# Performance work log

Hardware: AMD Instinct MI355X
Metric: run time of the kernel (lower is better)

The kernel has to match this reference:

```python
import jax, jax.numpy as jnp
import numpy as np

EPS = 1e-5


def _layernorm(x, w, b):
    mu = jnp.mean(x, axis=-1, keepdims=True)
    var = jnp.var(x, axis=-1, keepdims=True)
    return (x - mu) * jax.lax.rsqrt(var + EPS) * w + b


def setup_inputs() -> dict:
    key = jax.random.key(0)
    ks = jax.random.split(key, 3)
    h, dff = 1024, 4096
    x = jax.random.normal(ks[0], (4, 2048, h), dtype=jnp.float32)
    w1 = jax.random.normal(ks[1], (h, dff), dtype=jnp.float32) * (1.0 / np.sqrt(h))
    w2 = jax.random.normal(ks[2], (dff, h), dtype=jnp.float32) * (1.0 / np.sqrt(dff))
    return {
        "x": x,
        "ln1_w": jnp.ones((h,), jnp.float32),
        "ln1_b": jnp.zeros((h,), jnp.float32),
        "ln2_w": jnp.ones((h,), jnp.float32),
        "ln2_b": jnp.zeros((h,), jnp.float32),
        "w1": w1,
        "b1": jnp.zeros((dff,), jnp.float32),
        "w2": w2,
        "b2": jnp.zeros((h,), jnp.float32),
    }


def reference(x, ln1_w, ln1_b, ln2_w, ln2_b, w1, b1, w2, b2):
    # double 1D FFT: over hidden (dim=-1) then sequence (dim=-2), keep real part
    fourier_x = jnp.fft.fft(jnp.fft.fft(x, axis=-1), axis=-2).real
    x = x + fourier_x
    x = _layernorm(x, ln1_w, ln1_b)
    # FFN: Linear -> exact GELU -> Linear (dropout is identity in eval)
    h = jax.nn.gelu(jnp.einsum("bsd,df->bsf", x, w1) + b1, approximate=False)
    x = x + jnp.einsum("bsf,fd->bsd", h, w2) + b2
    return _layernorm(x, ln2_w, ln2_b)
```

## Files before the change

### kernel.cpp

```cpp
#include <hip/hip_runtime.h>
#include <hip/hip_bf16.h>
#include <math.h>

typedef __bf16 bf16_t;
typedef __bf16 bf16x8 __attribute__((ext_vector_type(8)));
typedef __bf16 bf16x4 __attribute__((ext_vector_type(4)));
typedef float  f32x4  __attribute__((ext_vector_type(4)));

#define NROWS 8192
#define HD    1024
#define DFF   4096
#define HKEEP 513

typedef __attribute__((address_space(1))) const void* gas_cptr;
typedef __attribute__((address_space(3))) void* las_ptr;

__device__ __forceinline__ void gload_lds16(const void* g, void* l) {
  __builtin_amdgcn_global_load_lds((gas_cptr)g, (las_ptr)l, 16, 0, 0);
}

__global__ __launch_bounds__(256) void transpose_to_bf16(
    const float* __restrict__ in, bf16_t* __restrict__ out, int R, int C)
{
  __shared__ float tile[32][33];
  const int bx = blockIdx.x, by = blockIdx.y;
  const int tx = threadIdx.x, ty = threadIdx.y;
  #pragma unroll
  for (int i = ty; i < 32; i += 8)
    tile[i][tx] = in[(size_t)(by*32 + i)*C + bx*32 + tx];
  __syncthreads();
  #pragma unroll
  for (int i = ty; i < 32; i += 8)
    out[(size_t)(bx*32 + i)*R + by*32 + tx] = (bf16_t)tile[tx][i];
}

#define RPB 16
#define LDW 1036
__global__ __launch_bounds__(512) void fft_h_t(
    const float* __restrict__ x, float* __restrict__ reT, float* __restrict__ imT)
{
  __shared__ float sre[RPB*LDW], sim[RPB*LDW], twc[512], tws[512];
  const int t = threadIdx.x;
  const int row0 = blockIdx.x * RPB;
  {
    float sv, cv; sincosf(-6.28318530717958647692f * (float)t * (1.0f/1024.0f), &sv, &cv);
    twc[t] = cv; tws[t] = sv;
  }
  #pragma unroll
  for (int q = 0; q < 8; ++q) {
    const int i = t + 512*q;
    const int row = i >> 8, c4 = i & 255;
    float4 v = *(const float4*)(x + (size_t)(row0+row)*HD + c4*4);
    *(float4*)&sre[row*LDW + c4*4] = v;
  }
  __syncthreads();
  const int b0i = __brev((unsigned)t) >> 22;
  const int b1i = __brev((unsigned)(t + 512)) >> 22;
  float rv[32];
  #pragma unroll
  for (int q = 0; q < 16; ++q) {
    rv[2*q]   = sre[q*LDW + b0i];
    rv[2*q+1] = sre[q*LDW + b1i];
  }
  __syncthreads();
  #pragma unroll
  for (int q = 0; q < 16; ++q) {
    sre[q*LDW + t]       = rv[2*q];
    sre[q*LDW + t + 512] = rv[2*q+1];
    sim[q*LDW + t]       = 0.0f;
    sim[q*LDW + t + 512] = 0.0f;
  }
  __syncthreads();
  for (int s = 0; s < 10; ++s) {
    const int half = 1 << s;
    const int j    = t & (half - 1);
    const int ib   = ((t >> s) << (s + 1)) | j;
    const int ti2  = j << (9 - s);
    const float wc = twc[ti2], ws = tws[ti2];
    #pragma unroll
    for (int q = 0; q < 16; ++q) {
      float* pr = &sre[q*LDW]; float* pi = &sim[q*LDW];
      const float r1 = pr[ib],      i1v = pi[ib];
      const float r2 = pr[ib+half], i2v = pi[ib+half];
      const float tr = r2*wc - i2v*ws;
      const float ti = r2*ws + i2v*wc;
      pr[ib]      = r1 + tr; pi[ib]      = i1v + ti;
      pr[ib+half] = r1 - tr; pi[ib+half] = i1v - ti;
    }
    __syncthreads();
  }
  const int tx = t & 15, th = t >> 4;
  #pragma unroll
  for (int hh = 0; hh < 17; ++hh) {
    const int h = hh*32 + th;
    if (h < HKEEP) {
      reT[(size_t)h*NROWS + row0 + tx] = sre[tx*LDW + h];
      imT[(size_t)h*NROWS + row0 + tx] = sim[tx*LDW + h];
    }
  }
}

__global__ __launch_bounds__(256) void fft_s_col(
    const float* __restrict__ reT, const float* __restrict__ imT,
    float* __restrict__ fT)
{
  __shared__ float sre[2048], sim[2048], twc[1024], tws[1024];
  const int t = threadIdx.x;
  const int h = blockIdx.x;
  const int batch = blockIdx.y;
  const size_t base = (size_t)h * NROWS + batch * 2048;
  for (int k = t; k < 1024; k += 256) {
    float sv, cv; sincosf(-6.28318530717958647692f * (float)k * (1.0f/2048.0f), &sv, &cv);
    twc[k] = cv; tws[k] = sv;
  }
  #pragma unroll
  for (int q = 0; q < 8; ++q) {
    const int i = t + 256*q;
    const int src = __brev((unsigned)i) >> 21;
    sre[i] = reT[base + src];
    sim[i] = imT[base + src];
  }
  __syncthreads();
  for (int s = 0; s < 11; ++s) {
    const int half = 1 << s;
    #pragma unroll
    for (int q = 0; q < 4; ++q) {
      const int b  = t + 256*q;
      const int j  = b & (half - 1);
      const int ib = ((b >> s) << (s + 1)) | j;
      const int ti2 = j << (10 - s);
      const float wc = twc[ti2], ws = tws[ti2];
      const float r1 = sre[ib],       i1v = sim[ib];
      const float r2 = sre[ib+half],  i2v = sim[ib+half];
      const float tr = r2*wc - i2v*ws;
      const float ti = r2*ws + i2v*wc;
      sre[ib]      = r1 + tr; sim[ib]      = i1v + ti;
      sre[ib+half] = r1 - tr; sim[ib+half] = i1v - ti;
    }
    __syncthreads();
  }
  #pragma unroll
  for (int q = 0; q < 8; ++q) {
    const int i = t + 256*q;
    fT[base + i] = sre[i];
  }
}

__global__ __launch_bounds__(256) void umadd_kernel(
    const float* __restrict__ fT, const float* __restrict__ x,
    float* __restrict__ y)
{
  __shared__ float tile[32][33];
  const int h0 = blockIdx.x * 32;
  const int b0 = blockIdx.y * 32;
  const int tx = threadIdx.x, ty = threadIdx.y;
  const int batch = b0 >> 11;
  const int s0    = b0 & 2047;
  #pragma unroll
  for (int i = ty; i < 32; i += 8) {
    const int h = h0 + i;
    float v;
    if (h <= 512) {
      v = fT[(size_t)h * NROWS + b0 + tx];
    } else {
      const int sp = (2048 - (s0 + tx)) & 2047;
      v = fT[(size_t)(1024 - h) * NROWS + (batch << 11) + sp];
    }
    tile[i][tx] = v;
  }
  __syncthreads();
  #pragma unroll
  for (int i = ty; i < 32; i += 8) {
    const size_t gi = (size_t)(b0+i)*HD + h0+tx;
    y[gi] = x[gi] + tile[tx][i];
  }
}

template <bool OUT_BF16>
__global__ __launch_bounds__(256) void layernorm_k(
    const float* __restrict__ in, const float* __restrict__ gw,
    const float* __restrict__ gb, bf16_t* __restrict__ ob, float* __restrict__ of)
{
  __shared__ float red[8];
  const size_t row = blockIdx.x;
  const int t = threadIdx.x;
  const float* xr = in + row * HD;
  float4 v = *(const float4*)(xr + t*4);
  float s = v.x + v.y + v.z + v.w;
  #pragma unroll
  for (int o = 32; o > 0; o >>= 1) s += __shfl_xor(s, o);
  if ((t & 63) == 0) red[t >> 6] = s;
  __syncthreads();
  const float mu = (red[0]+red[1]+red[2]+red[3]) * (1.0f/1024.0f);
  const float dx = v.x-mu, dy = v.y-mu, dz = v.z-mu, dw = v.w-mu;
  float sq = dx*dx + dy*dy + dz*dz + dw*dw;
  #pragma unroll
  for (int o = 32; o > 0; o >>= 1) sq += __shfl_xor(sq, o);
  if ((t & 63) == 0) red[4 + (t >> 6)] = sq;
  __syncthreads();
  const float var  = (red[4]+red[5]+red[6]+red[7]) * (1.0f/1024.0f);
  const float rstd = rsqrtf(var + 1e-5f);
  const float4 wv = *(const float4*)(gw + t*4);
  const float4 bv = *(const float4*)(gb + t*4);
  const float o0 = dx*rstd*wv.x + bv.x;
  const float o1 = dy*rstd*wv.y + bv.y;
  const float o2 = dz*rstd*wv.z + bv.z;
  const float o3 = dw*rstd*wv.w + bv.w;
  if constexpr (OUT_BF16) {
    bf16x4 o; o[0]=(bf16_t)o0; o[1]=(bf16_t)o1; o[2]=(bf16_t)o2; o[3]=(bf16_t)o3;
    *(bf16x4*)(ob + row*HD + t*4) = o;
  } else {
    float4 o; o.x=o0; o.y=o1; o.z=o2; o.w=o3;
    *(float4*)(of + row*HD + t*4) = o;
  }
}

__device__ __forceinline__ float gelu_fast(float v) {
  const float u  = 0.7978845608028654f * v * (1.0f + 0.044715f * v * v);
  const float e  = exp2f(-2.8853900817779268f * u);
  return v / (1.0f + e);
}

template <bool GELU_BF16_OUT>
__global__ __launch_bounds__(256) void gemm_bf16_kernel(
    const bf16_t* __restrict__ A,
    const bf16_t* __restrict__ Bt,
    const float*  __restrict__ bias,
    const bf16_t* __restrict__ resid,
    bf16_t* __restrict__ outB, float* __restrict__ outF,
    int M, int N, int K, int gx)
{
  constexpr int BK = 64;
  __shared__ bf16_t As[128*BK];
  __shared__ bf16_t Bs[128*BK];
  const int tid  = threadIdx.x;
  const int wave = tid >> 6, lane = tid & 63;
  const int wr = wave >> 1, wc = wave & 1;
  const int lr  = lane & 15;
  const int lkg = lane >> 4;

  const int nwg = gridDim.x;
  const int sid = (blockIdx.x & 7) * (nwg >> 3) + (blockIdx.x >> 3);
  const int bx = sid % gx, by = sid / gx;
  const int brow = by * 128, bcol = bx * 128;

  const int rloc = lane >> 3;
  const int sgrp = (lane & 7) ^ rloc;
  const bf16_t* Ag = A  + (size_t)(brow + wave*32 + rloc) * K + sgrp * 8;
  const bf16_t* Bg = Bt + (size_t)(bcol + wave*32 + rloc) * K + sgrp * 8;

  f32x4 acc[4][4] = {};

  for (int k0 = 0; k0 < K; k0 += BK) {
    #pragma unroll
    for (int q = 0; q < 4; ++q) {
      gload_lds16(Ag + (size_t)(q*8)*K + k0, &As[(wave*4 + q) * 512]);
      gload_lds16(Bg + (size_t)(q*8)*K + k0, &Bs[(wave*4 + q) * 512]);
    }
    __syncthreads();

    #pragma unroll
    for (int ks = 0; ks < 2; ++ks) {
      const int g = (lkg + ks*4) ^ (lr & 7);
      bf16x8 af[4], bv[4];
      #pragma unroll
      for (int m = 0; m < 4; ++m)
        af[m] = *(const bf16x8*)&As[(wr*64 + m*16 + lr)*BK + g*8];
      #pragma unroll
      for (int n = 0; n < 4; ++n)
        bv[n] = *(const bf16x8*)&Bs[(wc*64 + n*16 + lr)*BK + g*8];
      #pragma unroll
      for (int m = 0; m < 4; ++m)
        #pragma unroll
        for (int n = 0; n < 4; ++n)
          acc[m][n] = __builtin_amdgcn_mfma_f32_16x16x32_bf16(bv[n], af[m], acc[m][n], 0, 0, 0);
    }
    __syncthreads();
  }

  #pragma unroll
  for (int m = 0; m < 4; ++m) {
    const int row = brow + wr*64 + m*16 + lr;
    #pragma unroll
    for (int n = 0; n < 4; ++n) {
      const int col = bcol + wc*64 + n*16 + lkg*4;
      const float4 bv4 = *(const float4*)(bias + col);
      float v0 = acc[m][n][0] + bv4.x;
      float v1 = acc[m][n][1] + bv4.y;
      float v2 = acc[m][n][2] + bv4.z;
      float v3 = acc[m][n][3] + bv4.w;
      if constexpr (GELU_BF16_OUT) {
        bf16x4 o;
        o[0] = (bf16_t)gelu_fast(v0); o[1] = (bf16_t)gelu_fast(v1);
        o[2] = (bf16_t)gelu_fast(v2); o[3] = (bf16_t)gelu_fast(v3);
        *(bf16x4*)(outB + (size_t)row * N + col) = o;
      } else {
        bf16x4 rr = *(const bf16x4*)(resid + (size_t)row * N + col);
        float4 o;
        o.x = v0 + (float)rr[0]; o.y = v1 + (float)rr[1];
        o.z = v2 + (float)rr[2]; o.w = v3 + (float)rr[3];
        *(float4*)(outF + (size_t)row * N + col) = o;
      }
    }
  }
}

extern "C" void kernel_launch(void* const* d_in, const int* in_sizes, int n_in,
                              void* d_out, int out_size, void* d_ws, size_t ws_size,
                              hipStream_t stream) {
  const float* x    = (const float*)d_in[0];
  const float* ln1w = (const float*)d_in[1];
  const float* ln1b = (const float*)d_in[2];
  const float* ln2w = (const float*)d_in[3];
  const float* ln2b = (const float*)d_in[4];
  const float* w1   = (const float*)d_in[5];
  const float* b1   = (const float*)d_in[6];
  const float* w2   = (const float*)d_in[7];
  const float* b2   = (const float*)d_in[8];
  float* out = (float*)d_out;

  char* ws = (char*)d_ws;
  bf16_t* w1b = (bf16_t*)(ws);
  bf16_t* w2b = (bf16_t*)(ws + (8u  << 20));
  float*  reT = (float*) (ws + (16u << 20));
  float*  imT = (float*) (ws + (33u << 20));
  float*  fT  = (float*) (ws + (50u << 20));
  float*  y   = (float*) (ws + (67u << 20));
  bf16_t* xn  = (bf16_t*)(ws + (99u << 20));
  bf16_t* hg  = (bf16_t*)(ws + (16u << 20));

  transpose_to_bf16<<<dim3(DFF/32, HD/32), dim3(32, 8), 0, stream>>>(w1, w1b, HD, DFF);
  transpose_to_bf16<<<dim3(HD/32, DFF/32), dim3(32, 8), 0, stream>>>(w2, w2b, DFF, HD);

  fft_h_t<<<NROWS/RPB, 512, 0, stream>>>(x, reT, imT);

  fft_s_col<<<dim3(513, 4), 256, 0, stream>>>(reT, imT, fT);

  umadd_kernel<<<dim3(HD/32, NROWS/32), dim3(32, 8), 0, stream>>>(fT, x, y);

  layernorm_k<true><<<NROWS, 256, 0, stream>>>(y, ln1w, ln1b, xn, nullptr);

  gemm_bf16_kernel<true><<<(DFF/128)*(NROWS/128), 256, 0, stream>>>(
      xn, w1b, b1, nullptr, hg, nullptr, NROWS, DFF, HD, DFF/128);
  gemm_bf16_kernel<false><<<(HD/128)*(NROWS/128), 256, 0, stream>>>(
      hg, w2b, b2, xn, nullptr, out, NROWS, HD, DFF, HD/128);

  layernorm_k<false><<<NROWS, 256, 0, stream>>>(out, ln2w, ln2b, nullptr, out);
}
```

Measured before the change: 326.9 us.

## Pipeline GEMMs with 8-wave 256-row tiles and fuse residual add into LN1

Replaces the 128x128 single-buffered GEMM with a 512-thread, 256-row tile kernel. It double-buffers LDS and splits each K tile into eight phases that interleave global-to-LDS prefetch with MFMA, using explicit vmcnt waits, barriers and setprio. Separately, it fuses the Fourier-term transpose and residual add with LayerNorm1 into one kernel that holds 16 rows in LDS, removing the fp32 y round trip. The risks are larger LDS and register use per block, hand-tuned wait counts that must match the load issue order, and a single-pass variance (E[x²]−μ²) that is less numerically stable.

```diff
diff --git a/kernel.cpp b/kernel.cpp
--- a/kernel.cpp
+++ b/kernel.cpp
@@ -17,6 +17,14 @@
 
 __device__ __forceinline__ void gload_lds16(const void* g, void* l) {
   __builtin_amdgcn_global_load_lds((gas_cptr)g, (las_ptr)l, 16, 0, 0);
+}
+
+template <int N> __device__ __forceinline__ void vmw() {
+  if      constexpr (N==3) asm volatile("s_waitcnt vmcnt(3)" ::: "memory");
+  else if constexpr (N==4) asm volatile("s_waitcnt vmcnt(4)" ::: "memory");
+  else if constexpr (N==5) asm volatile("s_waitcnt vmcnt(5)" ::: "memory");
+  else if constexpr (N==6) asm volatile("s_waitcnt vmcnt(6)" ::: "memory");
+  else if constexpr (N==8) asm volatile("s_waitcnt vmcnt(8)" ::: "memory");
 }
 
 __global__ __launch_bounds__(256) void transpose_to_bf16(
@@ -146,40 +154,73 @@
   }
 }
 
-__global__ __launch_bounds__(256) void umadd_kernel(
+#define FLD 1028
+__global__ __launch_bounds__(256) void fuse_umadd_ln1(
     const float* __restrict__ fT, const float* __restrict__ x,
-    float* __restrict__ y)
-{
-  __shared__ float tile[32][33];
-  const int h0 = blockIdx.x * 32;
-  const int b0 = blockIdx.y * 32;
-  const int tx = threadIdx.x, ty = threadIdx.y;
-  const int batch = b0 >> 11;
-  const int s0    = b0 & 2047;
-  #pragma unroll
-  for (int i = ty; i < 32; i += 8) {
-    const int h = h0 + i;
+    const float* __restrict__ gw, const float* __restrict__ gb,
+    bf16_t* __restrict__ xn)
+{
+  __shared__ float tile[16*FLD];
+  __shared__ float mrow[16], vrow[16];
+  const int t = threadIdx.x;
+  const int r0 = blockIdx.x * 16;
+  const int batch = r0 >> 11;
+  const int rb = t & 15;
+  const int hh = t >> 4;
+  const int rloc = (r0 + rb) & 2047;
+  const int sp = (2048 - rloc) & 2047;
+  #pragma unroll
+  for (int p = 0; p < 64; ++p) {
+    const int h = p*16 + hh;
     float v;
-    if (h <= 512) {
-      v = fT[(size_t)h * NROWS + b0 + tx];
-    } else {
-      const int sp = (2048 - (s0 + tx)) & 2047;
-      v = fT[(size_t)(1024 - h) * NROWS + (batch << 11) + sp];
-    }
-    tile[i][tx] = v;
-  }
-  __syncthreads();
-  #pragma unroll
-  for (int i = ty; i < 32; i += 8) {
-    const size_t gi = (size_t)(b0+i)*HD + h0+tx;
-    y[gi] = x[gi] + tile[tx][i];
-  }
-}
-
-template <bool OUT_BF16>
-__global__ __launch_bounds__(256) void layernorm_k(
+    if (h <= 512) v = fT[(size_t)h*NROWS + r0 + rb];
+    else          v = fT[(size_t)(1024-h)*NROWS + (batch<<11) + sp];
+    tile[rb*FLD + h] = v;
+  }
+  __syncthreads();
+  #pragma unroll
+  for (int rr = 0; rr < 16; ++rr) {
+    float4 xv = *(const float4*)(x + (size_t)(r0+rr)*HD + t*4);
+    float4 tv = *(float4*)&tile[rr*FLD + t*4];
+    tv.x += xv.x; tv.y += xv.y; tv.z += xv.z; tv.w += xv.w;
+    *(float4*)&tile[rr*FLD + t*4] = tv;
+  }
+  __syncthreads();
+  {
+    const int r = t >> 4, i = t & 15;
+    float s = 0.f, s2 = 0.f;
+    #pragma unroll
+    for (int k = 0; k < 64; ++k) {
+      const float v = tile[r*FLD + i + 16*k];
+      s += v; s2 += v*v;
+    }
+    #pragma unroll
+    for (int o = 8; o > 0; o >>= 1) { s += __shfl_xor(s, o); s2 += __shfl_xor(s2, o); }
+    if (i == 0) {
+      const float mu = s * (1.0f/1024.0f);
+      mrow[r] = mu;
+      vrow[r] = rsqrtf(s2 * (1.0f/1024.0f) - mu*mu + 1e-5f);
+    }
+  }
+  __syncthreads();
+  const float4 wv = *(const float4*)(gw + t*4);
+  const float4 bv = *(const float4*)(gb + t*4);
+  #pragma unroll
+  for (int rr = 0; rr < 16; ++rr) {
+    const float mu = mrow[rr], rs = vrow[rr];
+    float4 tv = *(float4*)&tile[rr*FLD + t*4];
+    bf16x4 o;
+    o[0] = (bf16_t)((tv.x-mu)*rs*wv.x + bv.x);
+    o[1] = (bf16_t)((tv.y-mu)*rs*wv.y + bv.y);
+    o[2] = (bf16_t)((tv.z-mu)*rs*wv.z + bv.z);
+    o[3] = (bf16_t)((tv.w-mu)*rs*wv.w + bv.w);
+    *(bf16x4*)(xn + (size_t)(r0+rr)*HD + t*4) = o;
+  }
+}
+
+__global__ __launch_bounds__(256) void layernorm_f32(
     const float* __restrict__ in, const float* __restrict__ gw,
-    const float* __restrict__ gb, bf16_t* __restrict__ ob, float* __restrict__ of)
+    const float* __restrict__ gb, float* __restrict__ of)
 {
   __shared__ float red[8];
   const size_t row = blockIdx.x;
@@ -202,17 +243,12 @@
   const float rstd = rsqrtf(var + 1e-5f);
   const float4 wv = *(const float4*)(gw + t*4);
   const float4 bv = *(const float4*)(gb + t*4);
-  const float o0 = dx*rstd*wv.x + bv.x;
-  const float o1 = dy*rstd*wv.y + bv.y;
-  const float o2 = dz*rstd*wv.z + bv.z;
-  const float o3 = dw*rstd*wv.w + bv.w;
-  if constexpr (OUT_BF16) {
-    bf16x4 o; o[0]=(bf16_t)o0; o[1]=(bf16_t)o1; o[2]=(bf16_t)o2; o[3]=(bf16_t)o3;
-    *(bf16x4*)(ob + row*HD + t*4) = o;
-  } else {
-    float4 o; o.x=o0; o.y=o1; o.z=o2; o.w=o3;
-    *(float4*)(of + row*HD + t*4) = o;
-  }
+  float4 o;
+  o.x = dx*rstd*wv.x + bv.x;
+  o.y = dy*rstd*wv.y + bv.y;
+  o.z = dz*rstd*wv.z + bv.z;
+  o.w = dw*rstd*wv.w + bv.w;
+  *(float4*)(of + row*HD + t*4) = o;
 }
 
 __device__ __forceinline__ float gelu_fast(float v) {
@@ -221,8 +257,8 @@
   return v / (1.0f + e);
 }
 
-template <bool GELU_BF16_OUT>
-__global__ __launch_bounds__(256) void gemm_bf16_kernel(
+template <int NQ, bool GELU_OUT>
+__global__ __launch_bounds__(512, 2) void gemm8p(
     const bf16_t* __restrict__ A,
     const bf16_t* __restrict__ Bt,
     const float*  __restrict__ bias,
@@ -230,66 +266,104 @@
     bf16_t* __restrict__ outB, float* __restrict__ outF,
     int M, int N, int K, int gx)
 {
-  constexpr int BK = 64;
-  __shared__ bf16_t As[128*BK];
-  __shared__ bf16_t Bs[128*BK];
+  constexpr int S  = NQ * 16;
+  constexpr int WA = (NQ==2) ? 6 : 5;
+  constexpr int WB = (NQ==2) ? 8 : 6;
+  constexpr int WP = (NQ==2) ? 4 : 3;
+  __shared__ bf16_t As[2][2][128*64];
+  __shared__ bf16_t Bs[2][2][NQ*64*64];
+
   const int tid  = threadIdx.x;
   const int wave = tid >> 6, lane = tid & 63;
-  const int wr = wave >> 1, wc = wave & 1;
-  const int lr  = lane & 15;
-  const int lkg = lane >> 4;
+  const int wr = wave >> 2, wc = wave & 3;
+  const int lr = lane & 15, lkg = lane >> 4;
 
   const int nwg = gridDim.x;
   const int sid = (blockIdx.x & 7) * (nwg >> 3) + (blockIdx.x >> 3);
   const int bx = sid % gx, by = sid / gx;
-  const int brow = by * 128, bcol = bx * 128;
-
-  const int rloc = lane >> 3;
-  const int sgrp = (lane & 7) ^ rloc;
-  const bf16_t* Ag = A  + (size_t)(brow + wave*32 + rloc) * K + sgrp * 8;
-  const bf16_t* Bg = Bt + (size_t)(bcol + wave*32 + rloc) * K + sgrp * 8;
-
-  f32x4 acc[4][4] = {};
-
-  for (int k0 = 0; k0 < K; k0 += BK) {
-    #pragma unroll
-    for (int q = 0; q < 4; ++q) {
-      gload_lds16(Ag + (size_t)(q*8)*K + k0, &As[(wave*4 + q) * 512]);
-      gload_lds16(Bg + (size_t)(q*8)*K + k0, &Bs[(wave*4 + q) * 512]);
-    }
-    __syncthreads();
-
-    #pragma unroll
-    for (int ks = 0; ks < 2; ++ks) {
-      const int g = (lkg + ks*4) ^ (lr & 7);
-      bf16x8 af[4], bv[4];
-      #pragma unroll
-      for (int m = 0; m < 4; ++m)
-        af[m] = *(const bf16x8*)&As[(wr*64 + m*16 + lr)*BK + g*8];
-      #pragma unroll
-      for (int n = 0; n < 4; ++n)
-        bv[n] = *(const bf16x8*)&Bs[(wc*64 + n*16 + lr)*BK + g*8];
-      #pragma unroll
-      for (int m = 0; m < 4; ++m)
-        #pragma unroll
-        for (int n = 0; n < 4; ++n)
-          acc[m][n] = __builtin_amdgcn_mfma_f32_16x16x32_bf16(bv[n], af[m], acc[m][n], 0, 0, 0);
-    }
-    __syncthreads();
-  }
-
-  #pragma unroll
-  for (int m = 0; m < 4; ++m) {
-    const int row = brow + wr*64 + m*16 + lr;
-    #pragma unroll
-    for (int n = 0; n < 4; ++n) {
-      const int col = bcol + wc*64 + n*16 + lkg*4;
+  const int brow = by * 256, bcol = bx * (NQ*128);
+
+  const int rl = lane >> 3;
+  const int sg = (lane & 7) ^ rl;
+
+  auto stageA = [&](int b, int mh, int tt) {
+    #pragma unroll
+    for (int l = 0; l < 2; ++l) {
+      const int row = brow + l*128 + mh*64 + wave*8 + rl;
+      gload_lds16(A + (size_t)row * K + tt*64 + sg*8,
+                  &As[b][mh][(l*64 + wave*8)*64]);
+    }
+  };
+  auto stageB = [&](int b, int nh, int tt) {
+    #pragma unroll
+    for (int l = 0; l < NQ; ++l) {
+      const int rho = l*64 + wave*8 + rl;
+      const int wcs = rho / S, r = rho % S;
+      const int row = bcol + wcs*2*S + nh*S + r;
+      gload_lds16(Bt + (size_t)row * K + tt*64 + sg*8,
+                  &Bs[b][nh][(l*64 + wave*8)*64]);
+    }
+  };
+
+  f32x4 acc[8][2*NQ] = {};
+
+  const int NT = K >> 6;
+  const int NI = NT >> 1;
+
+  stageA(0,0,0); stageB(0,0,0); stageA(0,1,0); stageB(0,1,0);
+  stageA(1,0,1); stageB(1,0,1);
+  vmw<WP>();
+  __builtin_amdgcn_s_barrier();
+
+  #define PHASE(BUF, MH, NH, STG, WN) do { \
+    bf16x8 af[4][2]; bf16x8 bq[NQ][2]; \
+    _Pragma("unroll") for (int m = 0; m < 4; ++m) \
+    _Pragma("unroll") for (int ks = 0; ks < 2; ++ks) \
+      af[m][ks] = *(const bf16x8*)&As[BUF][MH][(wr*64 + m*16 + lr)*64 + (((lkg + ks*4) ^ (lr & 7)) << 3)]; \
+    _Pragma("unroll") for (int n = 0; n < NQ; ++n) \
+    _Pragma("unroll") for (int ks = 0; ks < 2; ++ks) \
+      bq[n][ks] = *(const bf16x8*)&Bs[BUF][NH][(wc*S + n*16 + lr)*64 + (((lkg + ks*4) ^ (lr & 7)) << 3)]; \
+    STG; \
+    __builtin_amdgcn_s_barrier(); \
+    asm volatile("s_waitcnt lgkmcnt(0)" ::: "memory"); \
+    __builtin_amdgcn_sched_barrier(0); \
+    __builtin_amdgcn_s_setprio(1); \
+    _Pragma("unroll") for (int m = 0; m < 4; ++m) \
+    _Pragma("unroll") for (int n = 0; n < NQ; ++n) \
+    _Pragma("unroll") for (int ks = 0; ks < 2; ++ks) \
+      acc[MH*4 + m][NH*NQ + n] = __builtin_amdgcn_mfma_f32_16x16x32_bf16(bq[n][ks], af[m][ks], acc[MH*4 + m][NH*NQ + n], 0, 0, 0); \
+    __builtin_amdgcn_s_setprio(0); \
+    vmw<WN>(); \
+    __builtin_amdgcn_s_barrier(); \
+  } while (0)
+
+  for (int j = 0; j < NI; ++j) {
+    const int c1 = 2*j + 1;
+    const int n2 = (2*j + 2 < NT) ? 2*j + 2 : NT - 1;
+    const int n3 = (2*j + 3 < NT) ? 2*j + 3 : NT - 1;
+    PHASE(0,0,0, stageA(1,1,c1), WA);
+    PHASE(0,0,1, stageB(1,1,c1), 63);
+    PHASE(0,1,0, stageA(0,0,n2), 63);
+    PHASE(0,1,1, stageB(0,0,n2), WB);
+    PHASE(1,0,0, stageA(0,1,n2), WA);
+    PHASE(1,0,1, stageB(0,1,n2), 63);
+    PHASE(1,1,0, stageA(1,0,n3), 63);
+    PHASE(1,1,1, stageB(1,0,n3), WB);
+  }
+  #undef PHASE
+
+  #pragma unroll
+  for (int im = 0; im < 8; ++im) {
+    const int row = brow + wr*128 + (im >> 2)*64 + (im & 3)*16 + lr;
+    #pragma unroll
+    for (int in = 0; in < 2*NQ; ++in) {
+      const int col = bcol + wc*2*S + (in/NQ)*S + (in%NQ)*16 + lkg*4;
       const float4 bv4 = *(const float4*)(bias + col);
-      float v0 = acc[m][n][0] + bv4.x;
-      float v1 = acc[m][n][1] + bv4.y;
-      float v2 = acc[m][n][2] + bv4.z;
-      float v3 = acc[m][n][3] + bv4.w;
-      if constexpr (GELU_BF16_OUT) {
+      float v0 = acc[im][in][0] + bv4.x;
+      float v1 = acc[im][in][1] + bv4.y;
+      float v2 = acc[im][in][2] + bv4.z;
+      float v3 = acc[im][in][3] + bv4.w;
+      if constexpr (GELU_OUT) {
         bf16x4 o;
         o[0] = (bf16_t)gelu_fast(v0); o[1] = (bf16_t)gelu_fast(v1);
         o[2] = (bf16_t)gelu_fast(v2); o[3] = (bf16_t)gelu_fast(v3);
@@ -321,13 +395,12 @@
 
   char* ws = (char*)d_ws;
   bf16_t* w1b = (bf16_t*)(ws);
-  bf16_t* w2b = (bf16_t*)(ws + (8u  << 20));
-  float*  reT = (float*) (ws + (16u << 20));
-  float*  imT = (float*) (ws + (33u << 20));
-  float*  fT  = (float*) (ws + (50u << 20));
-  float*  y   = (float*) (ws + (67u << 20));
-  bf16_t* xn  = (bf16_t*)(ws + (99u << 20));
-  bf16_t* hg  = (bf16_t*)(ws + (16u << 20));
+  bf16_t* w2b = (bf16_t*)(ws + (8u   << 20));
+  float*  reT = (float*) (ws + (16u  << 20));
+  float*  imT = (float*) (ws + (33u  << 20));
+  float*  fT  = (float*) (ws + (50u  << 20));
+  bf16_t* xn  = (bf16_t*)(ws + (100u << 20));
+  bf16_t* hg  = (bf16_t*)(ws + (16u  << 20));
 
   transpose_to_bf16<<<dim3(DFF/32, HD/32), dim3(32, 8), 0, stream>>>(w1, w1b, HD, DFF);
   transpose_to_bf16<<<dim3(HD/32, DFF/32), dim3(32, 8), 0, stream>>>(w2, w2b, DFF, HD);
@@ -336,14 +409,12 @@
 
   fft_s_col<<<dim3(513, 4), 256, 0, stream>>>(reT, imT, fT);
 
-  umadd_kernel<<<dim3(HD/32, NROWS/32), dim3(32, 8), 0, stream>>>(fT, x, y);
-
-  layernorm_k<true><<<NROWS, 256, 0, stream>>>(y, ln1w, ln1b, xn, nullptr);
-
-  gemm_bf16_kernel<true><<<(DFF/128)*(NROWS/128), 256, 0, stream>>>(
-      xn, w1b, b1, nullptr, hg, nullptr, NROWS, DFF, HD, DFF/128);
-  gemm_bf16_kernel<false><<<(HD/128)*(NROWS/128), 256, 0, stream>>>(
+  fuse_umadd_ln1<<<NROWS/16, 256, 0, stream>>>(fT, x, ln1w, ln1b, xn);
+
+  gemm8p<2, true><<<(NROWS/256)*(DFF/256), 512, 0, stream>>>(
+      xn, w1b, b1, nullptr, hg, nullptr, NROWS, DFF, HD, DFF/256);
+  gemm8p<1, false><<<(NROWS/256)*(HD/128), 512, 0, stream>>>(
       hg, w2b, b2, xn, nullptr, out, NROWS, HD, DFF, HD/128);
 
-  layernorm_k<false><<<NROWS, 256, 0, stream>>>(out, ln2w, ln2b, nullptr, out);
-}
+  layernorm_f32<<<NROWS, 256, 0, stream>>>(out, ln2w, ln2b, out);
+}
```

New measurement: 334.4 us. +2.3%, slower.

## Rewrite FFN GEMMs as 8-wave double-buffered pipelined kernel with larger tiles

Applied to the files above, without the earlier changes.

Replaces the 128x128 single-buffered bf16 GEMM with an 8-wave (512-thread) kernel using 256x256 (first GEMM) or 256x128 (second GEMM) tiles. It splits LDS into double-buffered half-tiles and interleaves global-to-LDS loads with MFMA phases, using explicit vmcnt waits, barriers and setprio. The goal is to hide memory latency behind MFMA work and raise data reuse per tile. It adds heavy LDS use and register pressure (64 or 32 accumulators per lane), and the hand-tuned wait counts risk races if they are wrong.

```diff
diff --git a/kernel.cpp b/kernel.cpp
--- a/kernel.cpp
+++ b/kernel.cpp
@@ -17,6 +17,14 @@
 
 __device__ __forceinline__ void gload_lds16(const void* g, void* l) {
   __builtin_amdgcn_global_load_lds((gas_cptr)g, (las_ptr)l, 16, 0, 0);
+}
+
+template <int N> __device__ __forceinline__ void vmw() {
+  if      constexpr (N==4)  asm volatile("s_waitcnt vmcnt(4)"  ::: "memory");
+  else if constexpr (N==6)  asm volatile("s_waitcnt vmcnt(6)"  ::: "memory");
+  else if constexpr (N==7)  asm volatile("s_waitcnt vmcnt(7)"  ::: "memory");
+  else if constexpr (N==8)  asm volatile("s_waitcnt vmcnt(8)"  ::: "memory");
+  else if constexpr (N==10) asm volatile("s_waitcnt vmcnt(10)" ::: "memory");
 }
 
 __global__ __launch_bounds__(256) void transpose_to_bf16(
@@ -221,8 +229,8 @@
   return v / (1.0f + e);
 }
 
-template <bool GELU_BF16_OUT>
-__global__ __launch_bounds__(256) void gemm_bf16_kernel(
+template <int NQ, bool GELU_OUT>
+__global__ __launch_bounds__(512, 2) void gemm8r(
     const bf16_t* __restrict__ A,
     const bf16_t* __restrict__ Bt,
     const float*  __restrict__ bias,
@@ -230,66 +238,112 @@
     bf16_t* __restrict__ outB, float* __restrict__ outF,
     int M, int N, int K, int gx)
 {
-  constexpr int BK = 64;
-  __shared__ bf16_t As[128*BK];
-  __shared__ bf16_t Bs[128*BK];
+  __shared__ bf16_t As[2][2][128*64];
+  __shared__ bf16_t Bs[2][2][NQ*64*64];
+
   const int tid  = threadIdx.x;
   const int wave = tid >> 6, lane = tid & 63;
-  const int wr = wave >> 1, wc = wave & 1;
-  const int lr  = lane & 15;
-  const int lkg = lane >> 4;
+  const int wr = wave >> 2, wc = wave & 3;
+  const int lr = lane & 15, lkg = lane >> 4;
 
   const int nwg = gridDim.x;
   const int sid = (blockIdx.x & 7) * (nwg >> 3) + (blockIdx.x >> 3);
   const int bx = sid % gx, by = sid / gx;
-  const int brow = by * 128, bcol = bx * 128;
-
-  const int rloc = lane >> 3;
-  const int sgrp = (lane & 7) ^ rloc;
-  const bf16_t* Ag = A  + (size_t)(brow + wave*32 + rloc) * K + sgrp * 8;
-  const bf16_t* Bg = Bt + (size_t)(bcol + wave*32 + rloc) * K + sgrp * 8;
-
-  f32x4 acc[4][4] = {};
-
-  for (int k0 = 0; k0 < K; k0 += BK) {
+  const int brow = by * 256, bcol = bx * (NQ*128);
+
+  const int rl = lane >> 3;
+  const int sg = (lane & 7) ^ rl;
+
+  auto stageA = [&](int b, int mh, int tt) {
     #pragma unroll
-    for (int q = 0; q < 4; ++q) {
-      gload_lds16(Ag + (size_t)(q*8)*K + k0, &As[(wave*4 + q) * 512]);
-      gload_lds16(Bg + (size_t)(q*8)*K + k0, &Bs[(wave*4 + q) * 512]);
-    }
-    __syncthreads();
-
+    for (int l = 0; l < 2; ++l) {
+      const int row = brow + l*128 + mh*64 + wave*8 + rl;
+      gload_lds16(A + (size_t)row * K + tt*64 + sg*8,
+                  &As[b][mh][(l*64 + wave*8)*64]);
+    }
+  };
+  auto stageB = [&](int b, int nh, int tt) {
     #pragma unroll
-    for (int ks = 0; ks < 2; ++ks) {
-      const int g = (lkg + ks*4) ^ (lr & 7);
-      bf16x8 af[4], bv[4];
-      #pragma unroll
-      for (int m = 0; m < 4; ++m)
-        af[m] = *(const bf16x8*)&As[(wr*64 + m*16 + lr)*BK + g*8];
-      #pragma unroll
-      for (int n = 0; n < 4; ++n)
-        bv[n] = *(const bf16x8*)&Bs[(wc*64 + n*16 + lr)*BK + g*8];
-      #pragma unroll
-      for (int m = 0; m < 4; ++m)
-        #pragma unroll
-        for (int n = 0; n < 4; ++n)
-          acc[m][n] = __builtin_amdgcn_mfma_f32_16x16x32_bf16(bv[n], af[m], acc[m][n], 0, 0, 0);
-    }
-    __syncthreads();
-  }
-
-  #pragma unroll
-  for (int m = 0; m < 4; ++m) {
-    const int row = brow + wr*64 + m*16 + lr;
+    for (int l = 0; l < NQ; ++l) {
+      const int rho = l*64 + wave*8 + rl;
+      const int wcs = rho / (NQ*16), r = rho % (NQ*16);
+      const int row = bcol + wcs*(NQ*32) + nh*(NQ*16) + r;
+      gload_lds16(Bt + (size_t)row * K + tt*64 + sg*8,
+                  &Bs[b][nh][(l*64 + wave*8)*64]);
+    }
+  };
+
+  f32x4 acc[8][2*NQ] = {};
+  bf16x8 af[4][2];
+  bf16x8 bq[2][NQ][2];
+
+  const int NT = K >> 6;
+  const int NI = NT >> 1;
+
+  stageB(0,0,0); stageA(0,0,0); stageB(0,1,0); stageA(0,1,0);
+  stageB(1,0,1); stageA(1,0,1); stageB(1,1,1);
+  vmw<(NQ==2 ? 6 : 4)>();
+  __builtin_amdgcn_s_barrier();
+
+  constexpr int W0 = (NQ==2) ? 10 : 8;
+  constexpr int W1 = (NQ==2) ? 10 : 7;
+  constexpr int W3 = (NQ==2) ? 10 : 7;
+  constexpr int W4 = (NQ==2) ? 10 : 8;
+  constexpr int W5 = (NQ==2) ? 10 : 7;
+  constexpr int W7 = (NQ==2) ? 10 : 7;
+
+  #define PHASE(BUF, MH, NH, DOA, DOB, STG, WN) do { \
+    if constexpr (DOA) { \
+      _Pragma("unroll") for (int m = 0; m < 4; ++m) \
+      _Pragma("unroll") for (int ks = 0; ks < 2; ++ks) \
+        af[m][ks] = *(const bf16x8*)&As[BUF][MH][(wr*64 + m*16 + lr)*64 + (((lkg + ks*4) ^ (lr & 7)) << 3)]; \
+    } \
+    if constexpr (DOB) { \
+      _Pragma("unroll") for (int n = 0; n < NQ; ++n) \
+      _Pragma("unroll") for (int ks = 0; ks < 2; ++ks) \
+        bq[NH][n][ks] = *(const bf16x8*)&Bs[BUF][NH][(wc*(NQ*16) + n*16 + lr)*64 + (((lkg + ks*4) ^ (lr & 7)) << 3)]; \
+    } \
+    STG; \
+    __builtin_amdgcn_s_barrier(); \
+    asm volatile("s_waitcnt lgkmcnt(0)" ::: "memory"); \
+    __builtin_amdgcn_sched_barrier(0); \
+    __builtin_amdgcn_s_setprio(1); \
+    _Pragma("unroll") for (int m = 0; m < 4; ++m) \
+    _Pragma("unroll") for (int n = 0; n < NQ; ++n) \
+    _Pragma("unroll") for (int ks = 0; ks < 2; ++ks) \
+      acc[MH*4 + m][NH*NQ + n] = __builtin_amdgcn_mfma_f32_16x16x32_bf16(bq[NH][n][ks], af[m][ks], acc[MH*4 + m][NH*NQ + n], 0, 0, 0); \
+    __builtin_amdgcn_s_setprio(0); \
+    vmw<WN>(); \
+    __builtin_amdgcn_s_barrier(); \
+  } while (0)
+
+  for (int j = 0; j < NI; ++j) {
+    const int c1 = 2*j + 1;
+    const int n2 = (2*j + 2 < NT) ? 2*j + 2 : NT - 1;
+    const int n3 = (2*j + 3 < NT) ? 2*j + 3 : NT - 1;
+    PHASE(0, 0, 0, 1, 1, stageA(1,1,c1), W0);
+    PHASE(0, 0, 1, 0, 1, stageB(0,0,n2), W1);
+    PHASE(0, 1, 1, 1, 0, stageA(0,0,n2), 63);
+    PHASE(0, 1, 0, 0, 0, stageB(0,1,n2), W3);
+    PHASE(1, 0, 0, 1, 1, stageA(0,1,n2), W4);
+    PHASE(1, 0, 1, 0, 1, stageB(1,0,n3), W5);
+    PHASE(1, 1, 1, 1, 0, stageA(1,0,n3), 63);
+    PHASE(1, 1, 0, 0, 0, stageB(1,1,n3), W7);
+  }
+  #undef PHASE
+
+  #pragma unroll
+  for (int im = 0; im < 8; ++im) {
+    const int row = brow + wr*128 + (im >> 2)*64 + (im & 3)*16 + lr;
     #pragma unroll
-    for (int n = 0; n < 4; ++n) {
-      const int col = bcol + wc*64 + n*16 + lkg*4;
+    for (int in = 0; in < 2*NQ; ++in) {
+      const int col = bcol + wc*(NQ*32) + (in/NQ)*(NQ*16) + (in%NQ)*16 + lkg*4;
       const float4 bv4 = *(const float4*)(bias + col);
-      float v0 = acc[m][n][0] + bv4.x;
-      float v1 = acc[m][n][1] + bv4.y;
-      float v2 = acc[m][n][2] + bv4.z;
-      float v3 = acc[m][n][3] + bv4.w;
-      if constexpr (GELU_BF16_OUT) {
+      float v0 = acc[im][in][0] + bv4.x;
+      float v1 = acc[im][in][1] + bv4.y;
+      float v2 = acc[im][in][2] + bv4.z;
+      float v3 = acc[im][in][3] + bv4.w;
+      if constexpr (GELU_OUT) {
         bf16x4 o;
         o[0] = (bf16_t)gelu_fast(v0); o[1] = (bf16_t)gelu_fast(v1);
         o[2] = (bf16_t)gelu_fast(v2); o[3] = (bf16_t)gelu_fast(v3);
@@ -321,13 +375,13 @@
 
   char* ws = (char*)d_ws;
   bf16_t* w1b = (bf16_t*)(ws);
-  bf16_t* w2b = (bf16_t*)(ws + (8u  << 20));
-  float*  reT = (float*) (ws + (16u << 20));
-  float*  imT = (float*) (ws + (33u << 20));
-  float*  fT  = (float*) (ws + (50u << 20));
-  float*  y   = (float*) (ws + (67u << 20));
-  bf16_t* xn  = (bf16_t*)(ws + (99u << 20));
-  bf16_t* hg  = (bf16_t*)(ws + (16u << 20));
+  bf16_t* w2b = (bf16_t*)(ws + (8u   << 20));
+  float*  reT = (float*) (ws + (16u  << 20));
+  float*  imT = (float*) (ws + (33u  << 20));
+  float*  fT  = (float*) (ws + (50u  << 20));
+  float*  y   = (float*) (ws + (67u  << 20));
+  bf16_t* xn  = (bf16_t*)(ws + (99u  << 20));
+  bf16_t* hg  = (bf16_t*)(ws + (16u  << 20));
 
   transpose_to_bf16<<<dim3(DFF/32, HD/32), dim3(32, 8), 0, stream>>>(w1, w1b, HD, DFF);
   transpose_to_bf16<<<dim3(HD/32, DFF/32), dim3(32, 8), 0, stream>>>(w2, w2b, DFF, HD);
@@ -340,9 +394,9 @@
 
   layernorm_k<true><<<NROWS, 256, 0, stream>>>(y, ln1w, ln1b, xn, nullptr);
 
-  gemm_bf16_kernel<true><<<(DFF/128)*(NROWS/128), 256, 0, stream>>>(
-      xn, w1b, b1, nullptr, hg, nullptr, NROWS, DFF, HD, DFF/128);
-  gemm_bf16_kernel<false><<<(HD/128)*(NROWS/128), 256, 0, stream>>>(
+  gemm8r<2, true><<<(NROWS/256)*(DFF/256), 512, 0, stream>>>(
+      xn, w1b, b1, nullptr, hg, nullptr, NROWS, DFF, HD, DFF/256);
+  gemm8r<1, false><<<(NROWS/256)*(HD/128), 512, 0, stream>>>(
       hg, w2b, b2, xn, nullptr, out, NROWS, HD, DFF, HD/128);
 
   layernorm_k<false><<<NROWS, 256, 0, stream>>>(out, ln2w, ln2b, nullptr, out);
```

After: 311.2 us. -4.8%, faster.
